# Kernel tuning notes

Measured on AMD Instinct MI355X. Metric: run time of the kernel, lower is better.

The kernel has to match this reference:

```python
import jax, jax.numpy as jnp
import numpy as np

B = 16384
NUM_DENSE = 13
NUM_SPARSE = 26
VOCAB = 100000
EMB = 64
MLP_DIMS = [512, 256, 64]
TOP_OUT = 256
TRIU_I, TRIU_J = np.triu_indices(NUM_SPARSE, k=1)  # 325 pairs


def setup_inputs() -> dict:
    key = jax.random.key(0)
    ks = jax.random.split(key, 12)
    inp = {}
    inp["dense_features"] = jax.random.normal(ks[0], (B, NUM_DENSE), dtype=jnp.float32)
    inp["sparse_features"] = jax.random.randint(ks[1], (B, NUM_SPARSE), 0, VOCAB, dtype=jnp.int64)
    # embedding tables, all same shape -> stacked [F, V, D]
    inp["tables"] = jax.random.normal(ks[2], (NUM_SPARSE, VOCAB, EMB), dtype=jnp.float32) * 0.01
    # bottom (dense) MLP: 13 -> 512 -> 256 -> 64, weights stored [in, out]
    dims = [NUM_DENSE] + MLP_DIMS
    for li in range(3):
        fan_in = dims[li]
        inp[f"W{li}"] = jax.random.normal(ks[3 + li], (dims[li], dims[li + 1]), dtype=jnp.float32) / np.sqrt(fan_in)
        inp[f"b{li}"] = jnp.zeros((dims[li + 1],), dtype=jnp.float32)
    # top MLP: (64 + 325) -> 256
    top_in = MLP_DIMS[-1] + NUM_SPARSE * (NUM_SPARSE - 1) // 2
    inp["Wt"] = jax.random.normal(ks[6], (top_in, TOP_OUT), dtype=jnp.float32) / np.sqrt(top_in)
    inp["bt"] = jnp.zeros((TOP_OUT,), dtype=jnp.float32)
    return inp


def reference(dense_features, sparse_features, tables, W0, b0, W1, b1, W2, b2, Wt, bt):
    # bottom MLP with ReLU after every layer (as in the torch Sequential)
    x = jax.nn.relu(dense_features @ W0 + b0)
    x = jax.nn.relu(x @ W1 + b1)
    dense_out = jax.nn.relu(x @ W2 + b2)  # [B, 64]

    # embedding gather: table f indexed by sparse_features[:, f] -> [B, F, D]
    emb = jax.vmap(lambda t, idx: t[idx], in_axes=(0, 1), out_axes=1)(tables, sparse_features)

    # pairwise dot interaction, upper triangle (i < j) -> [B, 325]
    gram = jnp.einsum('bid,bjd->bij', emb, emb)
    interact = gram[:, TRIU_I, TRIU_J]

    features = jnp.concatenate([dense_out, interact], axis=1)  # [B, 389]
    return features @ Wt + bt  # [B, 256]
```

## Files before the change

### kernel.cpp

```cpp
#include <hip/hip_runtime.h>
#include <hip/hip_bf16.h>


#define BATCH   16384
#define NSPARSE 26
#define VOCAB   100000
#define EMB     64
#define KTOP    416
#define KREAL   389
#define SPB     64
#define ASTR    424
#define X1STR   520
#define X2STR   264

typedef __attribute__((ext_vector_type(8)))  short bf16x8;
typedef __attribute__((ext_vector_type(4)))  short s16x4;
typedef __attribute__((ext_vector_type(4)))  float f32x4;
typedef __attribute__((ext_vector_type(16))) float f32x16;

__device__ inline void gload_lds16(const void* g, void* l) {
    __builtin_amdgcn_global_load_lds(
        (const __attribute__((address_space(1))) void*)g,
        (__attribute__((address_space(3))) void*)l, 16, 0, 0);
}

__device__ inline short f2bf(float x) {
    __hip_bfloat16 h = __float2bfloat16(x);
    return *reinterpret_cast<short*>(&h);
}

__global__ __launch_bounds__(256)
void prep_weights(const float* __restrict__ W0, const float* __restrict__ W1,
                  const float* __restrict__ W2, const float* __restrict__ Wt,
                  short* __restrict__ W0t, short* __restrict__ W1t,
                  short* __restrict__ W2t, short* __restrict__ Wtt)
{
    __shared__ float tile[32][36];
    int b = blockIdx.x, t = threadIdx.x;
    const float* src; short* dst; int K, N, Kpad, k0, n0;
    if (b < 16)        {              src = W0; dst = W0t; K = 13;  N = 512; Kpad = 32;  k0 = 0;           n0 = b * 32; }
    else if (b < 144)  { int i = b - 16;  src = W1; dst = W1t; K = 512; N = 256; Kpad = 512; k0 = (i >> 3) * 32; n0 = (i & 7) * 32; }
    else if (b < 160)  { int i = b - 144; src = W2; dst = W2t; K = 256; N = 64;  Kpad = 256; k0 = (i >> 1) * 32; n0 = (i & 1) * 32; }
    else               { int i = b - 160; src = Wt; dst = Wtt; K = 389; N = 256; Kpad = 416; k0 = (i >> 3) * 32; n0 = (i & 7) * 32; }

    int r = t >> 3, c4 = (t & 7) * 4;
    int gr = k0 + r;
    float4 v = make_float4(0.f, 0.f, 0.f, 0.f);
    if (gr < K) v = *(const float4*)(src + (size_t)gr * N + n0 + c4);
    tile[r][c4 + 0] = v.x; tile[r][c4 + 1] = v.y;
    tile[r][c4 + 2] = v.z; tile[r][c4 + 3] = v.w;
    __syncthreads();
    s16x4 o;
    #pragma unroll
    for (int j = 0; j < 4; ++j) o[j] = f2bf(tile[c4 + j][r]);
    *(s16x4*)&dst[(size_t)(n0 + r) * Kpad + k0 + c4] = o;
}

__global__ __launch_bounds__(512, 1)
void fused_all(const int* __restrict__ sparse, const float* __restrict__ tables,
               const float* __restrict__ D,
               const short* __restrict__ W0t, const float* __restrict__ b0,
               const short* __restrict__ W1t, const float* __restrict__ b1,
               const short* __restrict__ W2t, const float* __restrict__ b2,
               const short* __restrict__ Wtt, const float* __restrict__ bt,
               float* __restrict__ out)
{
    __shared__ __align__(16) char smem[157696];
    short* Ds   = (short*)(smem);
    short* As   = (short*)(smem + 4096);
    short* X1s  = (short*)(smem + 58368);
    short* X2s  = (short*)(smem + 58368);
    short* Bst0 = (short*)(smem + 124928);
    short* Bst1 = (short*)(smem + 141312);
    short* bufs[2] = {Bst0, Bst1};

    int tid = threadIdx.x;
    int w = tid >> 6, lane = tid & 63;
    int lr = lane & 15, lg = lane >> 4;
    int wr = w >> 2, wc = w & 3;
    int swz = (lg ^ (lr & 3)) * 8;
    int sbase = blockIdx.x * SPB;

    auto stage256 = [&](short* dstBuf, const short* W, int ldw, int k0) {
        #pragma unroll
        for (int rd = 0; rd < 2; ++rd) {
            int slot = rd * 512 + tid;
            int n = slot >> 2, kc = slot & 3;
            gload_lds16(W + (size_t)n * ldw + k0 + (kc ^ (n & 3)) * 8,
                        dstBuf + slot * 8);
        }
    };
    auto stage64 = [&](short* dstBuf, const short* W, int ldw, int k0) {
        if (tid < 256) {
            int n = tid >> 2, kc = tid & 3;
            gload_lds16(W + (size_t)n * ldw + k0 + (kc ^ (n & 3)) * 8,
                        dstBuf + tid * 8);
        }
    };

    for (int x = tid; x < SPB * 13; x += 512) {
        int r = x / 13, k = x - r * 13;
        Ds[r * 32 + k] = f2bf(D[(size_t)sbase * 13 + x]);
    }
    for (int x = tid; x < SPB * 19; x += 512) {
        int r = x / 19, k = 13 + (x - r * 19);
        Ds[r * 32 + k] = 0;
    }
    for (int x = tid; x < SPB * 27; x += 512) {
        int r = x / 27, c = x - r * 27;
        As[r * ASTR + KREAL + c] = 0;
    }
    __syncthreads();

    {
        int row = lane & 31, half = lane >> 5;
        int srow = (row < NSPARSE) ? row : 0;
        int idxv[8];
        #pragma unroll
        for (int li = 0; li < 8; ++li)
            idxv[li] = sparse[(sbase + w * 8 + li) * NSPARSE + srow];

        f32x4 Ca[4], Cb[4], Na[4], Nb[4];
        {
            const float* rp = tables + ((long)srow * VOCAB + idxv[0]) * EMB + half * 8;
            #pragma unroll
            for (int t = 0; t < 4; ++t) {
                Ca[t] = *(const f32x4*)(rp + t * 16);
                Cb[t] = *(const f32x4*)(rp + t * 16 + 4);
            }
        }
        #pragma unroll
        for (int li = 0; li < 8; ++li) {
            if (li < 7) {
                const float* rp = tables + ((long)srow * VOCAB + idxv[li + 1]) * EMB + half * 8;
                #pragma unroll
                for (int t = 0; t < 4; ++t) {
                    Na[t] = *(const f32x4*)(rp + t * 16);
                    Nb[t] = *(const f32x4*)(rp + t * 16 + 4);
                }
            }
            f32x16 acc = {};
            #pragma unroll
            for (int t = 0; t < 4; ++t) {
                bf16x8 f;
                #pragma unroll
                for (int j = 0; j < 4; ++j) f[j] = f2bf(Ca[t][j]);
                #pragma unroll
                for (int j = 0; j < 4; ++j) f[4 + j] = f2bf(Cb[t][j]);
                acc = __builtin_amdgcn_mfma_f32_32x32x16_bf16(f, f, acc, 0, 0, 0);
            }
            int c = row;
            if (c < NSPARSE) {
                #pragma unroll
                for (int reg = 0; reg < 16; ++reg) {
                    int r = (reg & 3) + 8 * (reg >> 2) + 4 * half;
                    if (r < c) {
                        int p = r * (2 * NSPARSE - r - 1) / 2 + (c - r - 1);
                        As[(w * 8 + li) * ASTR + 64 + p] = f2bf(acc[reg]);
                    }
                }
            }
            #pragma unroll
            for (int t = 0; t < 4; ++t) { Ca[t] = Na[t]; Cb[t] = Nb[t]; }
        }
    }

    {
        bf16x8 a0 = *(const bf16x8*)&Ds[(wr * 32 + lr) * 32 + lg * 8];
        bf16x8 a1 = *(const bf16x8*)&Ds[(wr * 32 + 16 + lr) * 32 + lg * 8];
        f32x4 acc[2][8] = {};
        #pragma unroll
        for (int ni = 0; ni < 8; ++ni) {
            bf16x8 b = *(const bf16x8*)(W0t + (size_t)(wc * 128 + ni * 16 + lr) * 32 + lg * 8);
            acc[0][ni] = __builtin_amdgcn_mfma_f32_16x16x32_bf16(a0, b, acc[0][ni], 0, 0, 0);
            acc[1][ni] = __builtin_amdgcn_mfma_f32_16x16x32_bf16(a1, b, acc[1][ni], 0, 0, 0);
        }
        #pragma unroll
        for (int ni = 0; ni < 8; ++ni) {
            int col = wc * 128 + ni * 16 + lr;
            float bv = b0[col];
            #pragma unroll
            for (int mi = 0; mi < 2; ++mi)
                #pragma unroll
                for (int j = 0; j < 4; ++j) {
                    int r = wr * 32 + mi * 16 + lg * 4 + j;
                    X1s[r * X1STR + col] = f2bf(fmaxf(acc[mi][ni][j] + bv, 0.f));
                }
        }
    }

    stage256(bufs[0], W1t, 512, 0);
    __syncthreads();
    {
        f32x4 acc[2][4] = {};
        int s = 0;
        for (int k0 = 0; k0 < 512; k0 += 32, s ^= 1) {
            if (k0 + 32 < 512) stage256(bufs[s ^ 1], W1t, 512, k0 + 32);
            bf16x8 a0 = *(const bf16x8*)&X1s[(wr * 32 + lr) * X1STR + k0 + lg * 8];
            bf16x8 a1 = *(const bf16x8*)&X1s[(wr * 32 + 16 + lr) * X1STR + k0 + lg * 8];
            #pragma unroll
            for (int ni = 0; ni < 4; ++ni) {
                int n = wc * 64 + ni * 16 + lr;
                bf16x8 b = *(const bf16x8*)&bufs[s][n * 32 + swz];
                acc[0][ni] = __builtin_amdgcn_mfma_f32_16x16x32_bf16(a0, b, acc[0][ni], 0, 0, 0);
                acc[1][ni] = __builtin_amdgcn_mfma_f32_16x16x32_bf16(a1, b, acc[1][ni], 0, 0, 0);
            }
            __syncthreads();
        }
        #pragma unroll
        for (int ni = 0; ni < 4; ++ni) {
            int col = wc * 64 + ni * 16 + lr;
            float bv = b1[col];
            #pragma unroll
            for (int mi = 0; mi < 2; ++mi)
                #pragma unroll
                for (int j = 0; j < 4; ++j) {
                    int r = wr * 32 + mi * 16 + lg * 4 + j;
                    X2s[r * X2STR + col] = f2bf(fmaxf(acc[mi][ni][j] + bv, 0.f));
                }
        }
    }

    stage64(bufs[0], W2t, 256, 0);
    __syncthreads();
    {
        f32x4 acc[2] = {};
        int s = 0;
        for (int k0 = 0; k0 < 256; k0 += 32, s ^= 1) {
            if (k0 + 32 < 256) stage64(bufs[s ^ 1], W2t, 256, k0 + 32);
            bf16x8 a0 = *(const bf16x8*)&X2s[(wr * 32 + lr) * X2STR + k0 + lg * 8];
            bf16x8 a1 = *(const bf16x8*)&X2s[(wr * 32 + 16 + lr) * X2STR + k0 + lg * 8];
            int n = wc * 16 + lr;
            bf16x8 b = *(const bf16x8*)&bufs[s][n * 32 + swz];
            acc[0] = __builtin_amdgcn_mfma_f32_16x16x32_bf16(a0, b, acc[0], 0, 0, 0);
            acc[1] = __builtin_amdgcn_mfma_f32_16x16x32_bf16(a1, b, acc[1], 0, 0, 0);
            __syncthreads();
        }
        int col = wc * 16 + lr;
        float bv = b2[col];
        #pragma unroll
        for (int mi = 0; mi < 2; ++mi)
            #pragma unroll
            for (int j = 0; j < 4; ++j) {
                int r = wr * 32 + mi * 16 + lg * 4 + j;
                As[r * ASTR + col] = f2bf(fmaxf(acc[mi][j] + bv, 0.f));
            }
    }

    stage256(bufs[0], Wtt, KTOP, 0);
    __syncthreads();
    {
        f32x4 acc[2][4] = {};
        int s = 0;
        for (int k0 = 0; k0 < KTOP; k0 += 32, s ^= 1) {
            if (k0 + 32 < KTOP) stage256(bufs[s ^ 1], Wtt, KTOP, k0 + 32);
            bf16x8 a0 = *(const bf16x8*)&As[(wr * 32 + lr) * ASTR + k0 + lg * 8];
            bf16x8 a1 = *(const bf16x8*)&As[(wr * 32 + 16 + lr) * ASTR + k0 + lg * 8];
            #pragma unroll
            for (int ni = 0; ni < 4; ++ni) {
                int n = wc * 64 + ni * 16 + lr;
                bf16x8 b = *(const bf16x8*)&bufs[s][n * 32 + swz];
                acc[0][ni] = __builtin_amdgcn_mfma_f32_16x16x32_bf16(a0, b, acc[0][ni], 0, 0, 0);
                acc[1][ni] = __builtin_amdgcn_mfma_f32_16x16x32_bf16(a1, b, acc[1][ni], 0, 0, 0);
            }
            __syncthreads();
        }
        #pragma unroll
        for (int ni = 0; ni < 4; ++ni) {
            int col = wc * 64 + ni * 16 + lr;
            float bv = bt[col];
            #pragma unroll
            for (int mi = 0; mi < 2; ++mi)
                #pragma unroll
                for (int j = 0; j < 4; ++j) {
                    int r = wr * 32 + mi * 16 + lg * 4 + j;
                    out[(size_t)(sbase + r) * 256 + col] = acc[mi][ni][j] + bv;
                }
        }
    }
}

extern "C" void kernel_launch(void* const* d_in, const int* in_sizes, int n_in,
                              void* d_out, int out_size, void* d_ws, size_t ws_size,
                              hipStream_t stream)
{
    const float* dense  = (const float*)d_in[0];
    const int*   sparse = (const int*)  d_in[1];
    const float* tables = (const float*)d_in[2];
    const float* W0     = (const float*)d_in[3];
    const float* b0     = (const float*)d_in[4];
    const float* W1     = (const float*)d_in[5];
    const float* b1     = (const float*)d_in[6];
    const float* W2     = (const float*)d_in[7];
    const float* b2     = (const float*)d_in[8];
    const float* Wt     = (const float*)d_in[9];
    const float* bt     = (const float*)d_in[10];
    float* out = (float*)d_out;

    char* ws = (char*)d_ws;
    short* W0t = (short*)(ws);
    short* W1t = (short*)(ws + 32768);
    short* W2t = (short*)(ws + 294912);
    short* Wtt = (short*)(ws + 327680);

    prep_weights<<<264, 256, 0, stream>>>(W0, W1, W2, Wt, W0t, W1t, W2t, Wtt);

    fused_all<<<BATCH / SPB, 512, 0, stream>>>(sparse, tables, dense,
                                               W0t, b0, W1t, b1, W2t, b2,
                                               Wtt, bt, out);
}
```

Baseline: 48.13 us.

## Triple-buffer weight staging with vmcnt waits and reorder MLP before interaction

Replaces the double-buffered weight staging loops, which used a full __syncthreads per K-step, with a three-buffer ring. Each step waits only on the older global-to-LDS loads (s_waitcnt vmcnt) and then issues a single barrier. The bottom MLP now runs before the embedding gather and interaction, so the As region can alias X1s and the shared-memory layout is reorganised. The goal is to cut barrier stalls and overlap weight loads with MFMA work. It relies on hand-counted vmcnt values, and any other outstanding global loads could make those counts wrong.

Result: faster. 45.47 us (-5.5%).

```diff
diff --git a/kernel.cpp b/kernel.cpp
--- a/kernel.cpp
+++ b/kernel.cpp
@@ -12,6 +12,8 @@
 #define ASTR    424
 #define X1STR   520
 #define X2STR   264
+
+#define WAIT_VMCNT(N) asm volatile("s_waitcnt vmcnt(" #N ")" ::: "memory")
 
 typedef __attribute__((ext_vector_type(8)))  short bf16x8;
 typedef __attribute__((ext_vector_type(4)))  short s16x4;
@@ -65,14 +67,14 @@
                const short* __restrict__ Wtt, const float* __restrict__ bt,
                float* __restrict__ out)
 {
-    __shared__ __align__(16) char smem[157696];
-    short* Ds   = (short*)(smem);
-    short* As   = (short*)(smem + 4096);
-    short* X1s  = (short*)(smem + 58368);
-    short* X2s  = (short*)(smem + 58368);
-    short* Bst0 = (short*)(smem + 124928);
-    short* Bst1 = (short*)(smem + 141312);
-    short* bufs[2] = {Bst0, Bst1};
+    __shared__ __align__(16) char smem[153600];
+    short* X1s = (short*)(smem);
+    short* As  = (short*)(smem);
+    short* X2s = (short*)(smem + 66560);
+    short* B0  = (short*)(smem + 100352);
+    short* B1  = (short*)(smem + 116736);
+    short* B2  = (short*)(smem + 133120);
+    short* Ds  = (short*)(smem + 149504);
 
     int tid = threadIdx.x;
     int w = tid >> 6, lane = tid & 63;
@@ -106,12 +108,89 @@
         int r = x / 19, k = 13 + (x - r * 19);
         Ds[r * 32 + k] = 0;
     }
+    __syncthreads();
+
+    {
+        bf16x8 a0 = *(const bf16x8*)&Ds[(wr * 32 + lr) * 32 + lg * 8];
+        bf16x8 a1 = *(const bf16x8*)&Ds[(wr * 32 + 16 + lr) * 32 + lg * 8];
+        f32x4 acc[2][8] = {};
+        #pragma unroll
+        for (int ni = 0; ni < 8; ++ni) {
+            bf16x8 b = *(const bf16x8*)(W0t + (size_t)(wc * 128 + ni * 16 + lr) * 32 + lg * 8);
+            acc[0][ni] = __builtin_amdgcn_mfma_f32_16x16x32_bf16(a0, b, acc[0][ni], 0, 0, 0);
+            acc[1][ni] = __builtin_amdgcn_mfma_f32_16x16x32_bf16(a1, b, acc[1][ni], 0, 0, 0);
+        }
+        #pragma unroll
+        for (int ni = 0; ni < 8; ++ni) {
+            int col = wc * 128 + ni * 16 + lr;
+            float bv = b0[col];
+            #pragma unroll
+            for (int mi = 0; mi < 2; ++mi)
+                #pragma unroll
+                for (int j = 0; j < 4; ++j) {
+                    int r = wr * 32 + mi * 16 + lg * 4 + j;
+                    X1s[r * X1STR + col] = f2bf(fmaxf(acc[mi][ni][j] + bv, 0.f));
+                }
+        }
+    }
+    __syncthreads();
+
+    {
+        stage256(B0, W1t, 512, 0);
+        stage256(B1, W1t, 512, 32);
+        short *bA = B0, *bB = B1, *bC = B2;
+        f32x4 acc[2][4] = {};
+        for (int k = 0; k < 15; ++k) {
+            WAIT_VMCNT(2);
+            __builtin_amdgcn_s_barrier();
+            __builtin_amdgcn_sched_barrier(0);
+            if (k + 2 < 16) stage256(bC, W1t, 512, (k + 2) * 32);
+            int k0 = k * 32;
+            bf16x8 a0 = *(const bf16x8*)&X1s[(wr * 32 + lr) * X1STR + k0 + lg * 8];
+            bf16x8 a1 = *(const bf16x8*)&X1s[(wr * 32 + 16 + lr) * X1STR + k0 + lg * 8];
+            #pragma unroll
+            for (int ni = 0; ni < 4; ++ni) {
+                int n = wc * 64 + ni * 16 + lr;
+                bf16x8 b = *(const bf16x8*)&bA[n * 32 + swz];
+                acc[0][ni] = __builtin_amdgcn_mfma_f32_16x16x32_bf16(a0, b, acc[0][ni], 0, 0, 0);
+                acc[1][ni] = __builtin_amdgcn_mfma_f32_16x16x32_bf16(a1, b, acc[1][ni], 0, 0, 0);
+            }
+            short* t = bA; bA = bB; bB = bC; bC = t;
+        }
+        WAIT_VMCNT(0);
+        __builtin_amdgcn_s_barrier();
+        __builtin_amdgcn_sched_barrier(0);
+        {
+            int k0 = 480;
+            bf16x8 a0 = *(const bf16x8*)&X1s[(wr * 32 + lr) * X1STR + k0 + lg * 8];
+            bf16x8 a1 = *(const bf16x8*)&X1s[(wr * 32 + 16 + lr) * X1STR + k0 + lg * 8];
+            #pragma unroll
+            for (int ni = 0; ni < 4; ++ni) {
+                int n = wc * 64 + ni * 16 + lr;
+                bf16x8 b = *(const bf16x8*)&bA[n * 32 + swz];
+                acc[0][ni] = __builtin_amdgcn_mfma_f32_16x16x32_bf16(a0, b, acc[0][ni], 0, 0, 0);
+                acc[1][ni] = __builtin_amdgcn_mfma_f32_16x16x32_bf16(a1, b, acc[1][ni], 0, 0, 0);
+            }
+        }
+        #pragma unroll
+        for (int ni = 0; ni < 4; ++ni) {
+            int col = wc * 64 + ni * 16 + lr;
+            float bv = b1[col];
+            #pragma unroll
+            for (int mi = 0; mi < 2; ++mi)
+                #pragma unroll
+                for (int j = 0; j < 4; ++j) {
+                    int r = wr * 32 + mi * 16 + lg * 4 + j;
+                    X2s[r * X2STR + col] = f2bf(fmaxf(acc[mi][ni][j] + bv, 0.f));
+                }
+        }
+    }
+    __syncthreads();
+
     for (int x = tid; x < SPB * 27; x += 512) {
         int r = x / 27, c = x - r * 27;
         As[r * ASTR + KREAL + c] = 0;
     }
-    __syncthreads();
-
     {
         int row = lane & 31, half = lane >> 5;
         int srow = (row < NSPARSE) ? row : 0;
@@ -166,75 +245,35 @@
     }
 
     {
-        bf16x8 a0 = *(const bf16x8*)&Ds[(wr * 32 + lr) * 32 + lg * 8];
-        bf16x8 a1 = *(const bf16x8*)&Ds[(wr * 32 + 16 + lr) * 32 + lg * 8];
-        f32x4 acc[2][8] = {};
-        #pragma unroll
-        for (int ni = 0; ni < 8; ++ni) {
-            bf16x8 b = *(const bf16x8*)(W0t + (size_t)(wc * 128 + ni * 16 + lr) * 32 + lg * 8);
-            acc[0][ni] = __builtin_amdgcn_mfma_f32_16x16x32_bf16(a0, b, acc[0][ni], 0, 0, 0);
-            acc[1][ni] = __builtin_amdgcn_mfma_f32_16x16x32_bf16(a1, b, acc[1][ni], 0, 0, 0);
-        }
-        #pragma unroll
-        for (int ni = 0; ni < 8; ++ni) {
-            int col = wc * 128 + ni * 16 + lr;
-            float bv = b0[col];
-            #pragma unroll
-            for (int mi = 0; mi < 2; ++mi)
-                #pragma unroll
-                for (int j = 0; j < 4; ++j) {
-                    int r = wr * 32 + mi * 16 + lg * 4 + j;
-                    X1s[r * X1STR + col] = f2bf(fmaxf(acc[mi][ni][j] + bv, 0.f));
-                }
-        }
-    }
-
-    stage256(bufs[0], W1t, 512, 0);
-    __syncthreads();
-    {
-        f32x4 acc[2][4] = {};
-        int s = 0;
-        for (int k0 = 0; k0 < 512; k0 += 32, s ^= 1) {
-            if (k0 + 32 < 512) stage256(bufs[s ^ 1], W1t, 512, k0 + 32);
-            bf16x8 a0 = *(const bf16x8*)&X1s[(wr * 32 + lr) * X1STR + k0 + lg * 8];
-            bf16x8 a1 = *(const bf16x8*)&X1s[(wr * 32 + 16 + lr) * X1STR + k0 + lg * 8];
-            #pragma unroll
-            for (int ni = 0; ni < 4; ++ni) {
-                int n = wc * 64 + ni * 16 + lr;
-                bf16x8 b = *(const bf16x8*)&bufs[s][n * 32 + swz];
-                acc[0][ni] = __builtin_amdgcn_mfma_f32_16x16x32_bf16(a0, b, acc[0][ni], 0, 0, 0);
-                acc[1][ni] = __builtin_amdgcn_mfma_f32_16x16x32_bf16(a1, b, acc[1][ni], 0, 0, 0);
-            }
-            __syncthreads();
-        }
-        #pragma unroll
-        for (int ni = 0; ni < 4; ++ni) {
-            int col = wc * 64 + ni * 16 + lr;
-            float bv = b1[col];
-            #pragma unroll
-            for (int mi = 0; mi < 2; ++mi)
-                #pragma unroll
-                for (int j = 0; j < 4; ++j) {
-                    int r = wr * 32 + mi * 16 + lg * 4 + j;
-                    X2s[r * X2STR + col] = f2bf(fmaxf(acc[mi][ni][j] + bv, 0.f));
-                }
-        }
-    }
-
-    stage64(bufs[0], W2t, 256, 0);
-    __syncthreads();
-    {
+        stage64(B0, W2t, 256, 0);
+        stage64(B1, W2t, 256, 32);
+        short *bA = B0, *bB = B1, *bC = B2;
         f32x4 acc[2] = {};
-        int s = 0;
-        for (int k0 = 0; k0 < 256; k0 += 32, s ^= 1) {
-            if (k0 + 32 < 256) stage64(bufs[s ^ 1], W2t, 256, k0 + 32);
+        for (int k = 0; k < 7; ++k) {
+            WAIT_VMCNT(1);
+            __builtin_amdgcn_s_barrier();
+            __builtin_amdgcn_sched_barrier(0);
+            if (k + 2 < 8) stage64(bC, W2t, 256, (k + 2) * 32);
+            int k0 = k * 32;
             bf16x8 a0 = *(const bf16x8*)&X2s[(wr * 32 + lr) * X2STR + k0 + lg * 8];
             bf16x8 a1 = *(const bf16x8*)&X2s[(wr * 32 + 16 + lr) * X2STR + k0 + lg * 8];
             int n = wc * 16 + lr;
-            bf16x8 b = *(const bf16x8*)&bufs[s][n * 32 + swz];
+            bf16x8 b = *(const bf16x8*)&bA[n * 32 + swz];
             acc[0] = __builtin_amdgcn_mfma_f32_16x16x32_bf16(a0, b, acc[0], 0, 0, 0);
             acc[1] = __builtin_amdgcn_mfma_f32_16x16x32_bf16(a1, b, acc[1], 0, 0, 0);
-            __syncthreads();
+            short* t = bA; bA = bB; bB = bC; bC = t;
+        }
+        WAIT_VMCNT(0);
+        __builtin_amdgcn_s_barrier();
+        __builtin_amdgcn_sched_barrier(0);
+        {
+            int k0 = 224;
+            bf16x8 a0 = *(const bf16x8*)&X2s[(wr * 32 + lr) * X2STR + k0 + lg * 8];
+            bf16x8 a1 = *(const bf16x8*)&X2s[(wr * 32 + 16 + lr) * X2STR + k0 + lg * 8];
+            int n = wc * 16 + lr;
+            bf16x8 b = *(const bf16x8*)&bA[n * 32 + swz];
+            acc[0] = __builtin_amdgcn_mfma_f32_16x16x32_bf16(a0, b, acc[0], 0, 0, 0);
+            acc[1] = __builtin_amdgcn_mfma_f32_16x16x32_bf16(a1, b, acc[1], 0, 0, 0);
         }
         int col = wc * 16 + lr;
         float bv = b2[col];
@@ -246,24 +285,44 @@
                 As[r * ASTR + col] = f2bf(fmaxf(acc[mi][j] + bv, 0.f));
             }
     }
-
-    stage256(bufs[0], Wtt, KTOP, 0);
-    __syncthreads();
-    {
+    __syncthreads();
+
+    {
+        stage256(B0, Wtt, KTOP, 0);
+        stage256(B1, Wtt, KTOP, 32);
+        short *bA = B0, *bB = B1, *bC = B2;
         f32x4 acc[2][4] = {};
-        int s = 0;
-        for (int k0 = 0; k0 < KTOP; k0 += 32, s ^= 1) {
-            if (k0 + 32 < KTOP) stage256(bufs[s ^ 1], Wtt, KTOP, k0 + 32);
+        for (int k = 0; k < 12; ++k) {
+            WAIT_VMCNT(2);
+            __builtin_amdgcn_s_barrier();
+            __builtin_amdgcn_sched_barrier(0);
+            if (k + 2 < 13) stage256(bC, Wtt, KTOP, (k + 2) * 32);
+            int k0 = k * 32;
             bf16x8 a0 = *(const bf16x8*)&As[(wr * 32 + lr) * ASTR + k0 + lg * 8];
             bf16x8 a1 = *(const bf16x8*)&As[(wr * 32 + 16 + lr) * ASTR + k0 + lg * 8];
             #pragma unroll
             for (int ni = 0; ni < 4; ++ni) {
                 int n = wc * 64 + ni * 16 + lr;
-                bf16x8 b = *(const bf16x8*)&bufs[s][n * 32 + swz];
+                bf16x8 b = *(const bf16x8*)&bA[n * 32 + swz];
                 acc[0][ni] = __builtin_amdgcn_mfma_f32_16x16x32_bf16(a0, b, acc[0][ni], 0, 0, 0);
                 acc[1][ni] = __builtin_amdgcn_mfma_f32_16x16x32_bf16(a1, b, acc[1][ni], 0, 0, 0);
             }
-            __syncthreads();
+            short* t = bA; bA = bB; bB = bC; bC = t;
+        }
+        WAIT_VMCNT(0);
+        __builtin_amdgcn_s_barrier();
+        __builtin_amdgcn_sched_barrier(0);
+        {
+            int k0 = 384;
+            bf16x8 a0 = *(const bf16x8*)&As[(wr * 32 + lr) * ASTR + k0 + lg * 8];
+            bf16x8 a1 = *(const bf16x8*)&As[(wr * 32 + 16 + lr) * ASTR + k0 + lg * 8];
+            #pragma unroll
+            for (int ni = 0; ni < 4; ++ni) {
+                int n = wc * 64 + ni * 16 + lr;
+                bf16x8 b = *(const bf16x8*)&bA[n * 32 + swz];
+                acc[0][ni] = __builtin_amdgcn_mfma_f32_16x16x32_bf16(a0, b, acc[0][ni], 0, 0, 0);
+                acc[1][ni] = __builtin_amdgcn_mfma_f32_16x16x32_bf16(a1, b, acc[1][ni], 0, 0, 0);
+            }
         }
         #pragma unroll
         for (int ni = 0; ni < 4; ++ni) {
```
